# Kernel optimization log

Measured on AMD Instinct MI355X. Metric: run time of the kernel, lower is better.

## Reference

```python
import jax, jax.numpy as jnp
import numpy as np

# Shapes hard-coded by the original module
B, C1, C2, S, K, H, E = 128, 128, 14, 14, 3, 256, 2  # batch, chan-split, chan-split, spatial, kernel, hidden, expand


def setup_inputs() -> dict:
    key = jax.random.key(0)
    k1, k2, k3 = jax.random.split(key, 3)
    x = jax.random.normal(k1, (B, C1 * C2, S), dtype=jnp.float32)
    w0 = jax.random.normal(k2, (H, E), dtype=jnp.float32)        # weights[0]
    w1 = jax.random.normal(k3, (C1, K, H), dtype=jnp.float32)    # weights[1]
    return {"x": x, "w0": w0, "w1": w1, "shift": 1}


def reference(x, w0, w1, shift):
    # reshape to (B, C1, C2, S); original torch treats it as (B, 1792, 14, 1)
    xr = x.reshape(B, C1, C2, S)
    # unfold((3,1), padding=(1,0)): 1D im2col along the S (=14) axis
    xp = jnp.pad(xr, ((0, 0), (0, 0), (0, 0), (1, 1)))
    # patches[b, j, n, i, m] = xp[b, j, n, m + i]  -> (B, C1, C2, K, S)
    patches = jnp.stack([xp[..., k:k + S] for k in range(K)], axis=3)
    # einsum 'ljnmi,jik->lnmk' (torch had m,i swapped via permute; fold it in)
    t4 = jnp.einsum('ljnim,jik->lnmk', patches, w1)   # (B, C2, S, H)
    # einsum 'kmlj,ji->kmlji': outer product with w0 along a new expand dim
    t5 = t4[..., None] * w0                            # (B, C2, S, H, E)
    t5 = jnp.roll(t5, shift, axis=1)                   # cyclic shift over C2
    t6 = jnp.transpose(t5, (0, 2, 3, 1, 4)).reshape(B, S, H, C2 * E)
    t6 = jnp.roll(t6, shift, axis=3)                   # cyclic shift over merged (C2*E)
    t6 = t6.reshape(B, S, H, C2, E).sum(axis=4)        # (B, S, H, C2)
    return jnp.transpose(t6, (0, 2, 3, 1))             # (B, H, C2, S) = (128, 256, 14, 14)
```

## Files before the change

kernel.cpp:

```cpp
#include <hip/hip_runtime.h>
#include <hip/hip_bf16.h>
#include <math.h>

#define B_   128
#define C1_  128
#define C2_  14
#define S_   14
#define K_   3
#define H_   256
#define E_   2

#define HT   64
#define NT   4
#define MT   13
#define CH   64
#define XSTR 72
#define BSTR 200
#define CROW 212

typedef unsigned short u16;
typedef unsigned int   u32;
typedef __attribute__((ext_vector_type(8))) short bf16x8;
typedef __attribute__((ext_vector_type(4))) float f32x4;

__device__ __forceinline__ u16 f2bf(float f) {
    u32 u = __float_as_uint(f);
    return (u16)((u + 0x7FFF + ((u >> 16) & 1)) >> 16);
}

__device__ __forceinline__ int decode_shift(const int* p) {
    int a = p[0];
    if (a >= -100 && a <= 100 && a != 0) return a;
    float f = __int_as_float(a);
    if (f >= -100.f && f <= 100.f && f == truncf(f) && f != 0.f) return (int)f;
    long long bits = ((long long)p[1] << 32) | (unsigned int)a;
    double d = __longlong_as_double(bits);
    if (d >= -100.0 && d <= 100.0 && d == trunc(d) && d != 0.0) return (int)d;
    return a;
}

__global__ __launch_bounds__(256) void cvt_kernel(const float* __restrict__ x,
                                                  const float* __restrict__ w1,
                                                  u16* __restrict__ xb,
                                                  u16* __restrict__ w1b) {
    const int NXq = (B_ * C1_ * C2_ * S_) / 4;
    const int NWq = (C1_ * K_ * H_) / 4;
    int q = blockIdx.x * 256 + threadIdx.x;
    float4 v; u16* dst;
    if (q < NXq)      { v = ((const float4*)x)[q];        dst = xb  + (size_t)q * 4; }
    else { int r = q - NXq; if (r >= NWq) return;
                       v = ((const float4*)w1)[r];        dst = w1b + (size_t)r * 4; }
    u32 lo = (u32)f2bf(v.x) | ((u32)f2bf(v.y) << 16);
    u32 hi = (u32)f2bf(v.z) | ((u32)f2bf(v.w) << 16);
    *(uint2*)dst = make_uint2(lo, hi);
}

template <bool PRE>
__global__ __launch_bounds__(256, 2) void fused_kernel(const void* __restrict__ xsrc,
                                                       const float* __restrict__ w0,
                                                       const void* __restrict__ wsrc,
                                                       const int* __restrict__ shift_p,
                                                       float* __restrict__ out) {
    __shared__ __align__(16) char lds[60160];
    u16*   xT = (u16*)lds;
    u16*   Bt = (u16*)(lds + 34560);
    float* Cl = (float*)lds;

    const int b    = blockIdx.x >> 2;
    const int h0   = (blockIdx.x & 3) * HT;
    const int t    = threadIdx.x;
    const int wave = t >> 6;
    const int lane = t & 63;
    const int quad = lane >> 4;
    const int l15  = lane & 15;

    f32x4 acc[4][NT];
#pragma unroll
    for (int i = 0; i < 4; ++i)
#pragma unroll
        for (int j = 0; j < NT; ++j) acc[i][j] = (f32x4){0.f, 0.f, 0.f, 0.f};

    for (int hf = 0; hf < 2; ++hf) {
        if (hf) __syncthreads();
        {
            const int oct = t >> 5, cs0 = t & 31;
            const int c1b = hf * CH + oct * 8;
#pragma unroll
            for (int i = 0; i < 7; ++i) {
                int cs = cs0 + 32 * i;
                if (cs < 196) {
                    int c2 = cs / 14, s = cs - c2 * 14;
                    u16 v[8];
                    if (PRE) {
                        const u16* xbp = (const u16*)xsrc + (size_t)b * (C1_ * 196);
#pragma unroll
                        for (int j = 0; j < 8; ++j) v[j] = xbp[(c1b + j) * 196 + cs];
                    } else {
                        const float* xf = (const float*)xsrc + (size_t)b * (C1_ * 196);
#pragma unroll
                        for (int j = 0; j < 8; ++j) v[j] = f2bf(xf[(c1b + j) * 196 + cs]);
                    }
                    u32 w[4];
#pragma unroll
                    for (int j = 0; j < 4; ++j) w[j] = (u32)v[2 * j] | ((u32)v[2 * j + 1] << 16);
                    *(uint4*)&xT[(c2 * 16 + s + 1) * XSTR + oct * 8] = make_uint4(w[0], w[1], w[2], w[3]);
                }
            }
            if (t < 224) {
                int c2 = t >> 4, r = t & 15;
                int p = (r & 1) ? 15 : 0, o = r >> 1;
                *(uint4*)&xT[(c2 * 16 + p) * XSTR + o * 8] = make_uint4(0, 0, 0, 0);
            }
        }
        {
            const int hl = t & 63, oc0 = t >> 6;
#pragma unroll
            for (int i = 0; i < 6; ++i) {
                int oc = oc0 + 4 * i;
                int kk = oc >> 3, o8 = (oc & 7) * 8;
                u16 v[8];
                if (PRE) {
                    const u16* wb = (const u16*)wsrc;
#pragma unroll
                    for (int j = 0; j < 8; ++j)
                        v[j] = wb[((hf * CH + o8 + j) * 3 + kk) * H_ + h0 + hl];
                } else {
                    const float* wf = (const float*)wsrc;
#pragma unroll
                    for (int j = 0; j < 8; ++j)
                        v[j] = f2bf(wf[((hf * CH + o8 + j) * 3 + kk) * H_ + h0 + hl]);
                }
                u32 w[4];
#pragma unroll
                for (int j = 0; j < 4; ++j) w[j] = (u32)v[2 * j] | ((u32)v[2 * j + 1] << 16);
                *(uint4*)&Bt[hl * BSTR + kk * 64 + o8] = make_uint4(w[0], w[1], w[2], w[3]);
            }
        }
        __syncthreads();

#pragma unroll
        for (int tt = 0; tt < 6; ++tt) {
            const int kk = tt >> 1;
            const int c1off = (tt & 1) * 32 + quad * 8;
            bf16x8 bf[NT];
#pragma unroll
            for (int nc = 0; nc < NT; ++nc)
                bf[nc] = *(const bf16x8*)&Bt[(nc * 16 + l15) * BSTR + tt * 32 + quad * 8];
#pragma unroll
            for (int mi = 0; mi < 4; ++mi) {
                int mt = wave + mi * 4;
                if (mt < MT) {
                    int r = mt * 16 + l15;
                    int c2 = r / 14, s = r - c2 * 14;
                    bf16x8 af = *(const bf16x8*)&xT[(c2 * 16 + s + kk) * XSTR + c1off];
#pragma unroll
                    for (int nc = 0; nc < NT; ++nc)
                        acc[mi][nc] = __builtin_amdgcn_mfma_f32_16x16x32_bf16(
                            af, bf[nc], acc[mi][nc], 0, 0, 0);
                }
            }
        }
    }

    __syncthreads();
#pragma unroll
    for (int mi = 0; mi < 4; ++mi) {
        int mt = wave + mi * 4;
        if (mt < MT) {
#pragma unroll
            for (int nc = 0; nc < NT; ++nc) {
                int hl = nc * 16 + l15;
                *(f32x4*)&Cl[hl * CROW + mt * 16 + quad * 4] = acc[mi][nc];
            }
        }
    }
    __syncthreads();

    const int shift = decode_shift(shift_p);
    const int hl = t >> 2, sub = t & 3;
    const int h = h0 + hl;
    int   c0[2]; float wv[2];
#pragma unroll
    for (int e = 0; e < 2; ++e) {
        int q = (e - shift) % 28; if (q < 0) q += 28;
        int np0 = q >> 1, ep = q & 1;
        int c = (np0 - shift) % 14; if (c < 0) c += 14;
        c0[e] = c;
        wv[e] = w0[h * 2 + ep];
    }
    const float* Crow = &Cl[hl * CROW];
    float* orow = out + (size_t)(b * H_ + h) * 196;
    int m = sub, n = 0;
    for (int i = 0; i < 49; ++i) {
        int cA = c0[0] + n; if (cA >= 14) cA -= 14;
        int cB = c0[1] + n; if (cB >= 14) cB -= 14;
        orow[n * 14 + m] = wv[0] * Crow[cA * 14 + m] + wv[1] * Crow[cB * 14 + m];
        m += 4; if (m >= 14) { m -= 14; ++n; }
    }
}

extern "C" void kernel_launch(void* const* d_in, const int* in_sizes, int n_in,
                              void* d_out, int out_size, void* d_ws, size_t ws_size,
                              hipStream_t stream) {
    const float* x     = (const float*)d_in[0];
    const float* w0    = (const float*)d_in[1];
    const float* w1    = (const float*)d_in[2];
    const int*   shift = (const int*)(n_in > 3 ? d_in[3] : d_in[n_in - 1]);
    for (int i = 0; i < n_in; ++i) {
        int sz = in_sizes[i];
        if (sz == B_ * C1_ * C2_ * S_)      x     = (const float*)d_in[i];
        else if (sz == H_ * E_)             w0    = (const float*)d_in[i];
        else if (sz == C1_ * K_ * H_)       w1    = (const float*)d_in[i];
        else if (sz == 1)                   shift = (const int*)d_in[i];
    }
    float* out = (float*)d_out;

    const size_t NX = (size_t)B_ * C1_ * C2_ * S_;
    const size_t NW = (size_t)C1_ * K_ * H_;
    if (ws_size >= (NX + NW) * sizeof(u16)) {
        u16* xb  = (u16*)d_ws;
        u16* w1b = xb + NX;
        const int NQ = (int)((NX + NW) / 4);
        cvt_kernel<<<(NQ + 255) / 256, 256, 0, stream>>>(x, w1, xb, w1b);
        fused_kernel<true><<<B_ * (H_ / HT), 256, 0, stream>>>(xb, w0, w1b, shift, out);
    } else {
        fused_kernel<false><<<B_ * (H_ / HT), 256, 0, stream>>>(x, w0, w1, shift, out);
    }
}
```

Before: 93.44 us.

## Pre-pack x and w1 into LDS-ready padded bf16 tiles in the convert kernel

The convert kernel now transposes x through shared memory into the padded, channel-interleaved row layout the GEMM kernel wants, and repacks w1 per h-group into contiguous tiles. The fused kernel then loads both operands as straight vectorized uint4 copies, with no scattered 2-byte gathers or index math. It also computes all 14 M-tiles over the padded rows, dropping the divide-by-14 addressing at the cost of some wasted MFMA work on pad rows, and writes the output with float4 stores. The fallback path without a workspace is replaced by simple fp32 kernels.

```diff
diff --git a/kernel.cpp b/kernel.cpp
--- a/kernel.cpp
+++ b/kernel.cpp
@@ -12,11 +12,10 @@
 
 #define HT   64
 #define NT   4
-#define MT   13
-#define CH   64
+#define XROWS 224
 #define XSTR 72
 #define BSTR 200
-#define CROW 212
+#define CROW 228
 
 typedef unsigned short u16;
 typedef unsigned int   u32;
@@ -41,33 +40,78 @@
 
 __global__ __launch_bounds__(256) void cvt_kernel(const float* __restrict__ x,
                                                   const float* __restrict__ w1,
-                                                  u16* __restrict__ xb,
-                                                  u16* __restrict__ w1b) {
-    const int NXq = (B_ * C1_ * C2_ * S_) / 4;
-    const int NWq = (C1_ * K_ * H_) / 4;
-    int q = blockIdx.x * 256 + threadIdx.x;
-    float4 v; u16* dst;
-    if (q < NXq)      { v = ((const float4*)x)[q];        dst = xb  + (size_t)q * 4; }
-    else { int r = q - NXq; if (r >= NWq) return;
-                       v = ((const float4*)w1)[r];        dst = w1b + (size_t)r * 4; }
-    u32 lo = (u32)f2bf(v.x) | ((u32)f2bf(v.y) << 16);
-    u32 hi = (u32)f2bf(v.z) | ((u32)f2bf(v.w) << 16);
-    *(uint2*)dst = make_uint2(lo, hi);
-}
-
-template <bool PRE>
-__global__ __launch_bounds__(256, 2) void fused_kernel(const void* __restrict__ xsrc,
+                                                  u16* __restrict__ xg,
+                                                  u16* __restrict__ wg) {
+    const int blk = blockIdx.x;
+    if (blk < 256) {
+        __shared__ u16 xl[64 * 200];
+        const int b = blk >> 1, hf = blk & 1;
+        const float4* src = (const float4*)(x + (size_t)(b * C1_ + hf * 64) * 196);
+        for (int q = threadIdx.x; q < 12544; q += 256) {
+            float4 v = src[q];
+            int c1l = q / 49, f4 = q - c1l * 49;
+            uint2 w;
+            w.x = (u32)f2bf(v.x) | ((u32)f2bf(v.y) << 16);
+            w.y = (u32)f2bf(v.z) | ((u32)f2bf(v.w) << 16);
+            *(uint2*)&xl[c1l * 200 + f4 * 4] = w;
+        }
+        __syncthreads();
+        u16* dst = xg + (size_t)(b * 2 + hf) * (XROWS * 64);
+        for (int idx = threadIdx.x; idx < 1792; idx += 256) {
+            int row = idx >> 3, o = idx & 7;
+            int c2 = row >> 4, p = row & 15;
+            uint4 val = make_uint4(0, 0, 0, 0);
+            if (p >= 1 && p <= 14) {
+                int cs = c2 * 14 + p - 1;
+                u16 v[8];
+#pragma unroll
+                for (int j = 0; j < 8; ++j) v[j] = xl[(o * 8 + j) * 200 + cs];
+                val.x = (u32)v[0] | ((u32)v[1] << 16);
+                val.y = (u32)v[2] | ((u32)v[3] << 16);
+                val.z = (u32)v[4] | ((u32)v[5] << 16);
+                val.w = (u32)v[6] | ((u32)v[7] << 16);
+            }
+            *(uint4*)&dst[idx * 8] = val;
+        }
+    } else {
+        const int base = (blk - 256) * 1536;
+        for (int ii = threadIdx.x; ii < 1536; ii += 256) {
+            int idx = base + ii;
+            int co = idx % 24;
+            int rest = idx / 24;
+            int hl = rest & 63;
+            int g2 = rest >> 6;
+            int hf = g2 & 1, g = g2 >> 1;
+            int kk = co >> 3, c1o = co & 7;
+            u16 v[8];
+#pragma unroll
+            for (int j = 0; j < 8; ++j) {
+                int c1 = hf * 64 + c1o * 8 + j;
+                v[j] = f2bf(w1[((size_t)c1 * K_ + kk) * H_ + g * 64 + hl]);
+            }
+            uint4 val;
+            val.x = (u32)v[0] | ((u32)v[1] << 16);
+            val.y = (u32)v[2] | ((u32)v[3] << 16);
+            val.z = (u32)v[4] | ((u32)v[5] << 16);
+            val.w = (u32)v[6] | ((u32)v[7] << 16);
+            *(uint4*)&wg[(size_t)idx * 8] = val;
+        }
+    }
+}
+
+__global__ __launch_bounds__(256, 2) void fused_kernel(const u16* __restrict__ xg,
                                                        const float* __restrict__ w0,
-                                                       const void* __restrict__ wsrc,
+                                                       const u16* __restrict__ wg,
                                                        const int* __restrict__ shift_p,
                                                        float* __restrict__ out) {
-    __shared__ __align__(16) char lds[60160];
+    __shared__ __align__(16) char lds[58368];
     u16*   xT = (u16*)lds;
-    u16*   Bt = (u16*)(lds + 34560);
+    u16*   Bt = (u16*)(lds + 32544);
     float* Cl = (float*)lds;
 
     const int b    = blockIdx.x >> 2;
-    const int h0   = (blockIdx.x & 3) * HT;
+    const int g    = blockIdx.x & 3;
+    const int h0   = g * HT;
     const int t    = threadIdx.x;
     const int wave = t >> 6;
     const int lane = t & 63;
@@ -83,57 +127,22 @@
     for (int hf = 0; hf < 2; ++hf) {
         if (hf) __syncthreads();
         {
-            const int oct = t >> 5, cs0 = t & 31;
-            const int c1b = hf * CH + oct * 8;
+            const uint4* src = (const uint4*)(xg + (size_t)(b * 2 + hf) * (XROWS * 64));
 #pragma unroll
             for (int i = 0; i < 7; ++i) {
-                int cs = cs0 + 32 * i;
-                if (cs < 196) {
-                    int c2 = cs / 14, s = cs - c2 * 14;
-                    u16 v[8];
-                    if (PRE) {
-                        const u16* xbp = (const u16*)xsrc + (size_t)b * (C1_ * 196);
-#pragma unroll
-                        for (int j = 0; j < 8; ++j) v[j] = xbp[(c1b + j) * 196 + cs];
-                    } else {
-                        const float* xf = (const float*)xsrc + (size_t)b * (C1_ * 196);
-#pragma unroll
-                        for (int j = 0; j < 8; ++j) v[j] = f2bf(xf[(c1b + j) * 196 + cs]);
-                    }
-                    u32 w[4];
-#pragma unroll
-                    for (int j = 0; j < 4; ++j) w[j] = (u32)v[2 * j] | ((u32)v[2 * j + 1] << 16);
-                    *(uint4*)&xT[(c2 * 16 + s + 1) * XSTR + oct * 8] = make_uint4(w[0], w[1], w[2], w[3]);
-                }
-            }
-            if (t < 224) {
-                int c2 = t >> 4, r = t & 15;
-                int p = (r & 1) ? 15 : 0, o = r >> 1;
-                *(uint4*)&xT[(c2 * 16 + p) * XSTR + o * 8] = make_uint4(0, 0, 0, 0);
+                int idx = t + 256 * i;
+                uint4 v = src[idx];
+                *(uint4*)&xT[(idx >> 3) * XSTR + (idx & 7) * 8] = v;
             }
         }
         {
-            const int hl = t & 63, oc0 = t >> 6;
+            const uint4* src = (const uint4*)(wg + (size_t)(g * 2 + hf) * (64 * 192));
 #pragma unroll
             for (int i = 0; i < 6; ++i) {
-                int oc = oc0 + 4 * i;
-                int kk = oc >> 3, o8 = (oc & 7) * 8;
-                u16 v[8];
-                if (PRE) {
-                    const u16* wb = (const u16*)wsrc;
-#pragma unroll
-                    for (int j = 0; j < 8; ++j)
-                        v[j] = wb[((hf * CH + o8 + j) * 3 + kk) * H_ + h0 + hl];
-                } else {
-                    const float* wf = (const float*)wsrc;
-#pragma unroll
-                    for (int j = 0; j < 8; ++j)
-                        v[j] = f2bf(wf[((hf * CH + o8 + j) * 3 + kk) * H_ + h0 + hl]);
-                }
-                u32 w[4];
-#pragma unroll
-                for (int j = 0; j < 4; ++j) w[j] = (u32)v[2 * j] | ((u32)v[2 * j + 1] << 16);
-                *(uint4*)&Bt[hl * BSTR + kk * 64 + o8] = make_uint4(w[0], w[1], w[2], w[3]);
+                int idx = t + 256 * i;
+                uint4 v = src[idx];
+                int hl = idx / 24, co = idx - hl * 24;
+                *(uint4*)&Bt[hl * BSTR + co * 8] = v;
             }
         }
         __syncthreads();
@@ -141,22 +150,21 @@
 #pragma unroll
         for (int tt = 0; tt < 6; ++tt) {
             const int kk = tt >> 1;
-            const int c1off = (tt & 1) * 32 + quad * 8;
-            bf16x8 bf[NT];
+            const int coff = (tt & 1) * 32 + quad * 8;
+            bf16x8 bfr[NT];
 #pragma unroll
             for (int nc = 0; nc < NT; ++nc)
-                bf[nc] = *(const bf16x8*)&Bt[(nc * 16 + l15) * BSTR + tt * 32 + quad * 8];
+                bfr[nc] = *(const bf16x8*)&Bt[(nc * 16 + l15) * BSTR + kk * 64 + coff];
 #pragma unroll
             for (int mi = 0; mi < 4; ++mi) {
                 int mt = wave + mi * 4;
-                if (mt < MT) {
+                if (mt < 14) {
                     int r = mt * 16 + l15;
-                    int c2 = r / 14, s = r - c2 * 14;
-                    bf16x8 af = *(const bf16x8*)&xT[(c2 * 16 + s + kk) * XSTR + c1off];
+                    bf16x8 af = *(const bf16x8*)&xT[(r + kk) * XSTR + coff];
 #pragma unroll
                     for (int nc = 0; nc < NT; ++nc)
                         acc[mi][nc] = __builtin_amdgcn_mfma_f32_16x16x32_bf16(
-                            af, bf[nc], acc[mi][nc], 0, 0, 0);
+                            af, bfr[nc], acc[mi][nc], 0, 0, 0);
                 }
             }
         }
@@ -166,7 +174,7 @@
 #pragma unroll
     for (int mi = 0; mi < 4; ++mi) {
         int mt = wave + mi * 4;
-        if (mt < MT) {
+        if (mt < 14) {
 #pragma unroll
             for (int nc = 0; nc < NT; ++nc) {
                 int hl = nc * 16 + l15;
@@ -179,7 +187,7 @@
     const int shift = decode_shift(shift_p);
     const int hl = t >> 2, sub = t & 3;
     const int h = h0 + hl;
-    int   c0[2]; float wv[2];
+    int c0[2]; float wv[2];
 #pragma unroll
     for (int e = 0; e < 2; ++e) {
         int q = (e - shift) % 28; if (q < 0) q += 28;
@@ -190,13 +198,77 @@
     }
     const float* Crow = &Cl[hl * CROW];
     float* orow = out + (size_t)(b * H_ + h) * 196;
-    int m = sub, n = 0;
-    for (int i = 0; i < 49; ++i) {
-        int cA = c0[0] + n; if (cA >= 14) cA -= 14;
-        int cB = c0[1] + n; if (cB >= 14) cB -= 14;
-        orow[n * 14 + m] = wv[0] * Crow[cA * 14 + m] + wv[1] * Crow[cB * 14 + m];
-        m += 4; if (m >= 14) { m -= 14; ++n; }
-    }
+#pragma unroll
+    for (int jj = 0; jj < 13; ++jj) {
+        int i = sub + 4 * jj;
+        if (i < 49) {
+            float tmp[4];
+#pragma unroll
+            for (int e4 = 0; e4 < 4; ++e4) {
+                int idx = 4 * i + e4;
+                int n = idx / 14, m = idx - n * 14;
+                int cA = c0[0] + n; if (cA >= 14) cA -= 14;
+                int cB = c0[1] + n; if (cB >= 14) cB -= 14;
+                tmp[e4] = wv[0] * Crow[cA * 16 + m] + wv[1] * Crow[cB * 16 + m];
+            }
+            *(float4*)&orow[4 * i] = make_float4(tmp[0], tmp[1], tmp[2], tmp[3]);
+        }
+    }
+}
+
+__global__ __launch_bounds__(256) void t4_fb(const float* __restrict__ x,
+                                             const float* __restrict__ w1,
+                                             float* __restrict__ t4) {
+    __shared__ float xl[C1_][16];
+    const int b = blockIdx.x / C2_, c2 = blockIdx.x % C2_, h = threadIdx.x;
+    for (int i = h; i < C1_ * S_; i += 256) {
+        int c1 = i / S_, s = i % S_;
+        xl[c1][s + 1] = x[((size_t)(b * C1_ + c1) * C2_ + c2) * S_ + s];
+    }
+    if (h < C1_) { xl[h][0] = 0.f; xl[h][15] = 0.f; }
+    __syncthreads();
+    float acc[S_];
+#pragma unroll
+    for (int s = 0; s < S_; ++s) acc[s] = 0.f;
+    for (int c1 = 0; c1 < C1_; ++c1) {
+        float wa = w1[(size_t)(c1 * K_ + 0) * H_ + h];
+        float wb = w1[(size_t)(c1 * K_ + 1) * H_ + h];
+        float wc = w1[(size_t)(c1 * K_ + 2) * H_ + h];
+#pragma unroll
+        for (int s = 0; s < S_; ++s)
+            acc[s] += wa * xl[c1][s] + wb * xl[c1][s + 1] + wc * xl[c1][s + 2];
+    }
+    size_t base = ((size_t)(b * H_ + h) * C2_ + c2) * S_;
+#pragma unroll
+    for (int s = 0; s < S_; ++s) t4[base + s] = acc[s];
+}
+__global__ __launch_bounds__(224) void out_fb(float* __restrict__ t4,
+                                              const float* __restrict__ w0,
+                                              const int* __restrict__ shift_p) {
+    const int tid = threadIdx.x;
+    const int m = tid % S_, hh = tid / S_;
+    const int b = blockIdx.x / 16, h = (blockIdx.x % 16) * 16 + hh;
+    const int shift = decode_shift(shift_p);
+    const size_t colbase = ((size_t)(b * H_ + h) * C2_) * S_ + m;
+    float tl[C2_];
+#pragma unroll
+    for (int c2 = 0; c2 < C2_; ++c2) tl[c2] = t4[colbase + (size_t)c2 * S_];
+    const float w0v[2] = { w0[h * 2 + 0], w0[h * 2 + 1] };
+    float r[C2_];
+#pragma unroll
+    for (int n = 0; n < C2_; ++n) {
+        float a = 0.f;
+#pragma unroll
+        for (int e = 0; e < 2; ++e) {
+            int q = (2 * n + e - shift) % 28; if (q < 0) q += 28;
+            int np = q >> 1, ep = q & 1;
+            int c2 = (np - shift) % 14; if (c2 < 0) c2 += 14;
+            a += tl[c2] * w0v[ep];
+        }
+        r[n] = a;
+    }
+#pragma unroll
+    for (int n = 0; n < C2_; ++n) t4[colbase + (size_t)n * S_] = r[n];
 }
 
 extern "C" void kernel_launch(void* const* d_in, const int* in_sizes, int n_in,
@@ -215,15 +287,15 @@
     }
     float* out = (float*)d_out;
 
-    const size_t NX = (size_t)B_ * C1_ * C2_ * S_;
-    const size_t NW = (size_t)C1_ * K_ * H_;
-    if (ws_size >= (NX + NW) * sizeof(u16)) {
-        u16* xb  = (u16*)d_ws;
-        u16* w1b = xb + NX;
-        const int NQ = (int)((NX + NW) / 4);
-        cvt_kernel<<<(NQ + 255) / 256, 256, 0, stream>>>(x, w1, xb, w1b);
-        fused_kernel<true><<<B_ * (H_ / HT), 256, 0, stream>>>(xb, w0, w1b, shift, out);
+    const size_t NXG = (size_t)B_ * 2 * XROWS * 64;
+    const size_t NWG = (size_t)4 * 2 * 64 * 192;
+    if (ws_size >= (NXG + NWG) * sizeof(u16)) {
+        u16* xg = (u16*)d_ws;
+        u16* wg = xg + NXG;
+        cvt_kernel<<<264, 256, 0, stream>>>(x, w1, xg, wg);
+        fused_kernel<<<B_ * 4, 256, 0, stream>>>(xg, w0, wg, shift, out);
     } else {
-        fused_kernel<false><<<B_ * (H_ / HT), 256, 0, stream>>>(x, w0, w1, shift, out);
-    }
-}
+        t4_fb<<<B_ * C2_, 256, 0, stream>>>(x, w1, out);
+        out_fb<<<B_ * 16, 224, 0, stream>>>(out, w0, shift);
+    }
+}
```

After: 105.4 us. 1.13x slower.
